# Optimization experiments

Measured on AMD Instinct MI355X. Metric: run time of the kernel, lower is better.

The kernel has to match this reference:

```python
import jax, jax.numpy as jnp
import numpy as np

N = 131072        # active input voxels (= output voxels for submanifold conv)
KVOL = 27         # 3x3x3 kernel volume
P = 65536         # neighbor pairs per kernel offset (regularized kernel map)
CIN = 64
COUT = 64


def setup_inputs() -> dict:
    key = jax.random.key(0)
    k1, k2, k3, k4, k5 = jax.random.split(key, 5)
    in_feats = jax.random.normal(k1, (N, CIN), dtype=jnp.float32)
    kernel = jax.random.normal(k2, (KVOL, CIN, COUT), dtype=jnp.float32) * (1.0 / np.sqrt(CIN * KVOL))
    bias_param = jax.random.normal(k3, (COUT,), dtype=jnp.float32)
    imap = jax.random.randint(k4, (KVOL, P), 0, N, dtype=jnp.int32)
    omap = jax.random.randint(k5, (KVOL, P), 0, N, dtype=jnp.int32)
    return {"in_feats": in_feats, "kernel": kernel, "bias_param": bias_param,
            "imap": imap, "omap": omap}


def reference(in_feats, kernel, bias_param, imap, omap):
    # Sparse 3D conv as gather -> per-offset GEMM -> scatter-add.
    # gathered: [KVOL, P, CIN]
    gathered = in_feats[imap]
    # per-offset GEMM: [KVOL, P, COUT]
    contrib = jnp.einsum('kpc,kco->kpo', gathered, kernel)
    out = jnp.zeros((N, COUT), dtype=in_feats.dtype)
    out = out.at[omap.reshape(-1)].add(contrib.reshape(-1, COUT))
    out = out + bias_param
    return out
```

## Files before the change

kernel.cpp:

```cpp
#include <hip/hip_runtime.h>
#include <hip/hip_bf16.h>
#include <stdint.h>

#define N_VOX 131072
#define KVOL  27
#define PPK   65536
#define CIN   64
#define COUT  64
#define TOT   (KVOL * PPK)
#define SORT_BLOCKS 864
#define GEMM_BLOCKS (KVOL * (PPK / 128))
#define NB    512

typedef __attribute__((ext_vector_type(8))) short short8;
typedef __attribute__((ext_vector_type(4))) float f32x4;

#define SCAN512(s, tid)                                       \
  for (int off = 1; off < 512; off <<= 1) {                   \
    int va_ = ((tid) >= off) ? s[(tid) - off] : 0;            \
    int vb_ = (((tid) + 256) >= off) ? s[(tid) + 256 - off] : 0; \
    __syncthreads();                                          \
    s[(tid)] += va_; s[(tid) + 256] += vb_;                   \
    __syncthreads();                                          \
  }

__device__ __forceinline__ void gl_lds16(const void* g, void* l) {
  __builtin_amdgcn_global_load_lds(
      (const __attribute__((address_space(1))) unsigned int*)g,
      (__attribute__((address_space(3))) unsigned int*)l,
      16, 0, 0);
}

__device__ __forceinline__ unsigned short f2bf(float f) {
  __hip_bfloat16 h = __float2bfloat16(f);
  return *reinterpret_cast<unsigned short*>(&h);
}


__global__ __launch_bounds__(256) void prep_hist_kernel(
    const float* __restrict__ in, unsigned short* __restrict__ inb,
    const float* __restrict__ w, unsigned short* __restrict__ wt,
    const int* __restrict__ omap, int* __restrict__ counts, int do_sort) {
  int b = blockIdx.x;
  if (do_sort) {
    if (b < SORT_BLOCKS) {
      __shared__ unsigned int hist[NB];
      int tid = threadIdx.x;
      hist[tid] = 0; hist[tid + 256] = 0;
      __syncthreads();
      int e0 = (b * 256 + tid) * 8;
      int4 o0 = *(const int4*)(omap + e0);
      int4 o1 = *(const int4*)(omap + e0 + 4);
      atomicAdd(&hist[(unsigned)o0.x >> 8], 1u);
      atomicAdd(&hist[(unsigned)o0.y >> 8], 1u);
      atomicAdd(&hist[(unsigned)o0.z >> 8], 1u);
      atomicAdd(&hist[(unsigned)o0.w >> 8], 1u);
      atomicAdd(&hist[(unsigned)o1.x >> 8], 1u);
      atomicAdd(&hist[(unsigned)o1.y >> 8], 1u);
      atomicAdd(&hist[(unsigned)o1.z >> 8], 1u);
      atomicAdd(&hist[(unsigned)o1.w >> 8], 1u);
      __syncthreads();
      counts[(size_t)b * NB + tid]       = (int)hist[tid];
      counts[(size_t)b * NB + tid + 256] = (int)hist[tid + 256];
      return;
    }
    b -= SORT_BLOCKS;
  }
  if (b < 4096) {
    int i = b * 256 + threadIdx.x;
    const float4* in4 = (const float4*)in;
    float4 f0 = in4[2 * i], f1 = in4[2 * i + 1];
    union { unsigned short u[8]; short8 v; } r;
    r.u[0] = f2bf(f0.x); r.u[1] = f2bf(f0.y); r.u[2] = f2bf(f0.z); r.u[3] = f2bf(f0.w);
    r.u[4] = f2bf(f1.x); r.u[5] = f2bf(f1.y); r.u[6] = f2bf(f1.z); r.u[7] = f2bf(f1.w);
    ((short8*)inb)[i] = r.v;
  } else {
    int k = b - 4096;
    const float* wk = w + k * CIN * COUT;
    unsigned short* wtk = wt + k * CIN * COUT;
    for (int idx = threadIdx.x; idx < CIN * COUT; idx += 256) {
      int c = idx >> 6, o = idx & 63;
      wtk[o * 64 + c] = f2bf(wk[idx]);
    }
  }
}


__global__ __launch_bounds__(256) void scan_blocks_kernel(
    const int* __restrict__ counts, int* __restrict__ blockbase,
    int* __restrict__ totals) {
  __shared__ int s[256];
  int b = blockIdx.x, t = threadIdx.x;
  int c0 = 0, c1 = 0, c2 = 0, c3 = 0;
  if (t < 216) {
    c0 = counts[(size_t)(4 * t + 0) * NB + b];
    c1 = counts[(size_t)(4 * t + 1) * NB + b];
    c2 = counts[(size_t)(4 * t + 2) * NB + b];
    c3 = counts[(size_t)(4 * t + 3) * NB + b];
  }
  int sum = c0 + c1 + c2 + c3;
  s[t] = sum; __syncthreads();
  for (int off = 1; off < 256; off <<= 1) {
    int v = (t >= off) ? s[t - off] : 0;
    __syncthreads();
    s[t] += v;
    __syncthreads();
  }
  int excl = s[t] - sum;
  int* brow = blockbase + (size_t)b * SORT_BLOCKS;
  if (t < 216) {
    brow[t * 4]     = excl;
    brow[t * 4 + 1] = excl + c0;
    brow[t * 4 + 2] = excl + c0 + c1;
    brow[t * 4 + 3] = excl + c0 + c1 + c2;
  }
  if (t == 255) totals[b] = s[255];
}


__global__ __launch_bounds__(256) void scatter_kernel(
    const int* __restrict__ omap, const int* __restrict__ blockbase,
    const int* __restrict__ totals, unsigned int* __restrict__ pairs) {
  __shared__ int ts[NB];
  __shared__ unsigned int gb[NB];
  __shared__ unsigned int cur[NB];
  int b = blockIdx.x, tid = threadIdx.x;
  int t0 = totals[tid], t1 = totals[tid + 256];
  ts[tid] = t0; ts[tid + 256] = t1;
  __syncthreads();
  SCAN512(ts, tid);
  gb[tid]       = (unsigned)(ts[tid] - t0 +
                    blockbase[(size_t)tid * SORT_BLOCKS + b]);
  gb[tid + 256] = (unsigned)(ts[tid + 256] - t1 +
                    blockbase[(size_t)(tid + 256) * SORT_BLOCKS + b]);
  cur[tid] = 0; cur[tid + 256] = 0;
  __syncthreads();
  int e0 = (b * 256 + tid) * 8;
  int4 o0 = *(const int4*)(omap + e0);
  int4 o1 = *(const int4*)(omap + e0 + 4);
  unsigned int key[8] = {(unsigned)o0.x, (unsigned)o0.y, (unsigned)o0.z, (unsigned)o0.w,
                         (unsigned)o1.x, (unsigned)o1.y, (unsigned)o1.z, (unsigned)o1.w};
#pragma unroll
  for (int i = 0; i < 8; i++) {
    unsigned int bk = key[i] >> 8;
    unsigned int r = atomicAdd(&cur[bk], 1u);
    unsigned int pos = gb[bk] + r;
    pairs[pos] = (((unsigned)(e0 + i)) << 8) | (key[i] & 255u);
  }
}


__global__ __launch_bounds__(256) void refine_kernel(
    const unsigned int* __restrict__ pairs, const int* __restrict__ totals,
    int* __restrict__ islotf, int* __restrict__ ofs, int* __restrict__ cnt) {
  __shared__ int ts[NB];
  __shared__ unsigned int hist[256];
  __shared__ unsigned int scn[256];
  __shared__ unsigned int cur[256];
  int b = blockIdx.x, t = threadIdx.x;
  int t0 = totals[t], t1 = totals[t + 256];
  ts[t] = t0; ts[t + 256] = t1;
  hist[t] = 0;
  __syncthreads();
  SCAN512(ts, t);
  __shared__ int sb_s, n_s;
  if (t == 0) { n_s = totals[b]; sb_s = ts[b] - n_s; }
  __syncthreads();
  int sb = sb_s, n = n_s;

  for (int i = t; i < n; i += 256)
    atomicAdd(&hist[pairs[sb + i] & 255u], 1u);
  __syncthreads();
  unsigned int h = hist[t];
  scn[t] = h;
  __syncthreads();
  for (int off = 1; off < 256; off <<= 1) {
    unsigned int v = (t >= off) ? scn[t - off] : 0;
    __syncthreads();
    scn[t] += v;
    __syncthreads();
  }
  unsigned int excl = scn[t] - h;
  ofs[b * 256 + t] = sb + (int)excl;
  cnt[b * 256 + t] = (int)h;
  cur[t] = excl;
  __syncthreads();
  for (int i = t; i < n; i += 256) {
    unsigned int v = pairs[sb + i];
    unsigned int r = atomicAdd(&cur[v & 255u], 1u);
    islotf[v >> 8] = sb + (int)r;
  }
}


__global__ __launch_bounds__(256) void spconv_store_kernel(
    const unsigned short* __restrict__ inb,
    const unsigned short* __restrict__ wt,
    const int* __restrict__ imap,
    const int* __restrict__ islotf,
    unsigned short* __restrict__ contrib) {
  __shared__ __align__(16) char smem[24576];
  short* A_lds = (short*)smem;
  short* B_lds = (short*)(smem + 16384);
  short* C_sh  = (short*)smem;
  __shared__ int perm_s[128];

  int bid = blockIdx.x;
  int k = bid >> 9;
  int pbase = (bid & 511) * 128;
  int tid = threadIdx.x;
  int wave = tid >> 6, lane = tid & 63;
  int m = lane & 15, q = lane >> 4;

  const int* imk = imap + k * PPK;
  const unsigned short* wtk = wt + k * 4096;

  if (tid < 128) perm_s[tid] = islotf[k * PPK + pbase + tid];

#pragma unroll
  for (int i = 0; i < 2; i++) {
    int id = wave * 2 + i;
    int t = id >> 1, s = id & 1;
    const unsigned short* g = wtk + (t * 16 + m) * 64 + s * 32 + q * 8;
    gl_lds16(g, &B_lds[(t * 128 + s * 64) * 8]);
  }
#pragma unroll
  for (int j = 0; j < 2; j++) {
    int r = wave * 2 + j;
    int row = imk[pbase + r * 16 + m];
    const unsigned short* g0 = inb + row * 64 + q * 8;
    gl_lds16(g0,      &A_lds[(r * 128)      * 8]);
    gl_lds16(g0 + 32, &A_lds[(r * 128 + 64) * 8]);
  }
  __syncthreads();

  const short8* Af = (const short8*)A_lds;
  const short8* Bf = (const short8*)B_lds;

  short8 a[2][2], b[4][2];
#pragma unroll
  for (int r2 = 0; r2 < 2; r2++) {
    int r = wave * 2 + r2;
#pragma unroll
    for (int s = 0; s < 2; s++) a[r2][s] = Af[r * 128 + s * 64 + lane];
  }
#pragma unroll
  for (int t = 0; t < 4; t++)
#pragma unroll
    for (int s = 0; s < 2; s++) b[t][s] = Bf[t * 128 + s * 64 + lane];

  __syncthreads();

  f32x4 acc[2][4];
#pragma unroll
  for (int r2 = 0; r2 < 2; r2++)
#pragma unroll
    for (int t = 0; t < 4; t++) {
      f32x4 c = {0.f, 0.f, 0.f, 0.f};
      c = __builtin_amdgcn_mfma_f32_16x16x32_bf16(a[r2][0], b[t][0], c, 0, 0, 0);
      c = __builtin_amdgcn_mfma_f32_16x16x32_bf16(a[r2][1], b[t][1], c, 0, 0, 0);
      acc[r2][t] = c;
    }

#pragma unroll
  for (int r2 = 0; r2 < 2; r2++) {
    int pl = (wave * 2 + r2) * 16 + q * 4;
#pragma unroll
    for (int t = 0; t < 4; t++)
#pragma unroll
      for (int reg = 0; reg < 4; reg++)
        C_sh[(pl + reg) * 72 + t * 16 + m] = (short)f2bf(acc[r2][t][reg]);
  }
  __syncthreads();

#pragma unroll
  for (int i = 0; i < 4; i++) {
    int id = i * 256 + tid;
    int row = id >> 3, ch = (id & 7) * 8;
    short8 v = *(const short8*)&C_sh[row * 72 + ch];
    *((short8*)&contrib[(size_t)perm_s[row] * 64 + ch]) = v;
  }
}


__global__ __launch_bounds__(256) void reduce_kernel(
    const unsigned short* __restrict__ contrib,
    const int* __restrict__ ofs,
    const int* __restrict__ cnt,
    const float* __restrict__ bias,
    float* __restrict__ out) {
  int row = blockIdx.x * 4 + (threadIdx.x >> 6);
  int lane = threadIdx.x & 63;
  int rg = lane >> 3, ch = (lane & 7) * 8;
  int s = ofs[row], n = cnt[row];

  float acc[8];
#pragma unroll
  for (int i = 0; i < 8; i++) acc[i] = 0.f;

  int j = rg;
  for (; j + 8 < n; j += 16) {
    short8 v0 = __builtin_nontemporal_load((const short8*)&contrib[(size_t)(s + j) * 64 + ch]);
    short8 v1 = __builtin_nontemporal_load((const short8*)&contrib[(size_t)(s + j + 8) * 64 + ch]);
#pragma unroll
    for (int i = 0; i < 8; i++)
      acc[i] += __uint_as_float((unsigned int)(unsigned short)v0[i] << 16);
#pragma unroll
    for (int i = 0; i < 8; i++)
      acc[i] += __uint_as_float((unsigned int)(unsigned short)v1[i] << 16);
  }
  if (j < n) {
    short8 v0 = __builtin_nontemporal_load((const short8*)&contrib[(size_t)(s + j) * 64 + ch]);
#pragma unroll
    for (int i = 0; i < 8; i++)
      acc[i] += __uint_as_float((unsigned int)(unsigned short)v0[i] << 16);
  }

#pragma unroll
  for (int mask = 8; mask < 64; mask <<= 1)
#pragma unroll
    for (int i = 0; i < 8; i++) acc[i] += __shfl_xor(acc[i], mask, 64);

  if (rg == 0) {
    float4 b0 = *(const float4*)(bias + ch);
    float4 b1 = *(const float4*)(bias + ch + 4);
    float4 r0 = {acc[0] + b0.x, acc[1] + b0.y, acc[2] + b0.z, acc[3] + b0.w};
    float4 r1 = {acc[4] + b1.x, acc[5] + b1.y, acc[6] + b1.z, acc[7] + b1.w};
    *(float4*)(out + (size_t)row * 64 + ch) = r0;
    *(float4*)(out + (size_t)row * 64 + ch + 4) = r1;
  }
}


__global__ __launch_bounds__(256) void init_out_kernel(float* __restrict__ out,
                                                       const float* __restrict__ bias) {
  int i = blockIdx.x * blockDim.x + threadIdx.x;
  float4 b = *(const float4*)(bias + ((i * 4) & 63));
  ((float4*)out)[i] = b;
}

__global__ __launch_bounds__(256) void spconv_atomic_kernel(
    const unsigned short* __restrict__ inb,
    const unsigned short* __restrict__ wt,
    const int* __restrict__ imap, const int* __restrict__ omap,
    float* __restrict__ out) {
  __shared__ __align__(16) short A_lds[128 * 64];
  __shared__ __align__(16) short B_lds[64 * 64];

  int bid = blockIdx.x;
  int k = bid >> 9;
  int pbase = (bid & 511) * 128;
  int tid = threadIdx.x;
  int wave = tid >> 6, lane = tid & 63;
  int m = lane & 15, q = lane >> 4;

  const int* imk = imap + k * PPK;
  const int* omk = omap + k * PPK;
  const unsigned short* wtk = wt + k * 4096;

#pragma unroll
  for (int i = 0; i < 2; i++) {
    int id = wave * 2 + i;
    int t = id >> 1, s = id & 1;
    const unsigned short* g = wtk + (t * 16 + m) * 64 + s * 32 + q * 8;
    gl_lds16(g, &B_lds[(t * 128 + s * 64) * 8]);
  }
#pragma unroll
  for (int j = 0; j < 2; j++) {
    int r = wave * 2 + j;
    int row = imk[pbase + r * 16 + m];
    const unsigned short* g0 = inb + row * 64 + q * 8;
    gl_lds16(g0,      &A_lds[(r * 128)      * 8]);
    gl_lds16(g0 + 32, &A_lds[(r * 128 + 64) * 8]);
  }
  __syncthreads();

  const short8* Af = (const short8*)A_lds;
  const short8* Bf = (const short8*)B_lds;
  short8 a[2][2], b[4][2];
#pragma unroll
  for (int r2 = 0; r2 < 2; r2++) {
    int r = wave * 2 + r2;
#pragma unroll
    for (int s = 0; s < 2; s++) a[r2][s] = Af[r * 128 + s * 64 + lane];
  }
#pragma unroll
  for (int t = 0; t < 4; t++)
#pragma unroll
    for (int s = 0; s < 2; s++) b[t][s] = Bf[t * 128 + s * 64 + lane];

  f32x4 acc[2][4];
#pragma unroll
  for (int r2 = 0; r2 < 2; r2++)
#pragma unroll
    for (int t = 0; t < 4; t++) {
      f32x4 c = {0.f, 0.f, 0.f, 0.f};
      c = __builtin_amdgcn_mfma_f32_16x16x32_bf16(a[r2][0], b[t][0], c, 0, 0, 0);
      c = __builtin_amdgcn_mfma_f32_16x16x32_bf16(a[r2][1], b[t][1], c, 0, 0, 0);
      acc[r2][t] = c;
    }

  int orow[2][4];
#pragma unroll
  for (int r2 = 0; r2 < 2; r2++) {
    int pr = pbase + (wave * 2 + r2) * 16 + q * 4;
#pragma unroll
    for (int reg = 0; reg < 4; reg++) orow[r2][reg] = omk[pr + reg];
  }
#pragma unroll
  for (int r2 = 0; r2 < 2; r2++)
#pragma unroll
    for (int t = 0; t < 4; t++)
#pragma unroll
      for (int reg = 0; reg < 4; reg++)
        atomicAdd(out + (size_t)orow[r2][reg] * 64 + t * 16 + m, acc[r2][t][reg]);
}


extern "C" void kernel_launch(void* const* d_in, const int* in_sizes, int n_in,
                              void* d_out, int out_size, void* d_ws, size_t ws_size,
                              hipStream_t stream) {
  const float* in_feats = (const float*)d_in[0];
  const float* kern     = (const float*)d_in[1];
  const float* bias     = (const float*)d_in[2];
  const int*   imap     = (const int*)d_in[3];
  const int*   omap     = (const int*)d_in[4];
  float* out = (float*)d_out;

  char* ws = (char*)d_ws;
  size_t off = 0;
  auto alloc = [&](size_t bytes) { size_t o = off; off = (off + bytes + 255) & ~(size_t)255; return o; };

  size_t o_inb   = alloc((size_t)N_VOX * CIN * 2);
  size_t o_wt    = alloc((size_t)KVOL * CIN * COUT * 2);
  size_t o_cts   = alloc((size_t)NB * SORT_BLOCKS * 4);
  size_t o_bb    = alloc((size_t)NB * SORT_BLOCKS * 4);
  size_t o_tot   = alloc((size_t)NB * 4);
  size_t o_islot = alloc((size_t)TOT * 4);
  size_t o_ctb   = alloc((size_t)TOT * 64 * 2);
  size_t needed = off;

  unsigned short* inb = (unsigned short*)(ws + o_inb);
  unsigned short* wt  = (unsigned short*)(ws + o_wt);
  int* counts    = (int*)(ws + o_cts);
  int* blockbase = (int*)(ws + o_bb);
  int* totals    = (int*)(ws + o_tot);
  int* islotf    = (int*)(ws + o_islot);
  unsigned short* ctb = (unsigned short*)(ws + o_ctb);
  unsigned int* pairs = (unsigned int*)(ws + o_ctb);
  int* ofs = (int*)(ws + o_cts);
  int* cnt = ofs + N_VOX;

  bool fast = (ws_size >= needed);

  if (fast) {
    prep_hist_kernel<<<SORT_BLOCKS + 4096 + KVOL, 256, 0, stream>>>(
        in_feats, inb, kern, wt, omap, counts, 1);
    scan_blocks_kernel<<<NB, 256, 0, stream>>>(counts, blockbase, totals);
    scatter_kernel<<<SORT_BLOCKS, 256, 0, stream>>>(omap, blockbase, totals, pairs);
    refine_kernel<<<NB, 256, 0, stream>>>(pairs, totals, islotf, ofs, cnt);
    spconv_store_kernel<<<GEMM_BLOCKS, 256, 0, stream>>>(inb, wt, imap, islotf, ctb);
    reduce_kernel<<<N_VOX / 4, 256, 0, stream>>>(ctb, ofs, cnt, bias, out);
  } else {
    prep_hist_kernel<<<4096 + KVOL, 256, 0, stream>>>(
        in_feats, inb, kern, wt, omap, nullptr, 0);
    init_out_kernel<<<(N_VOX * COUT / 4) / 256, 256, 0, stream>>>(out, bias);
    spconv_atomic_kernel<<<GEMM_BLOCKS, 256, 0, stream>>>(inb, wt, imap, omap, out);
  }
}
```

Measured before the change: 258.0 us.

## Fuse counting-sort stages into one cooperative kernel with grid syncs

Merges the four sort-related launches (histogram+convert, block scan, scatter, refine) into a single cooperative kernel of 512 persistent blocks separated by grid.sync barriers. The goal is to remove per-launch overhead and inter-kernel gaps, and to compute the bucket prefix sums once per block instead of recomputing them in separate kernels. In exchange, grid-stride loops run with fewer blocks than before, so the histogram, convert and scatter phases have less parallelism. Grid-wide barriers also add their own cost, and the cooperative launch requires all 512 blocks to be co-resident.

Result: slower. 475.4 us (+84.2%).

```diff
diff --git a/kernel.cpp b/kernel.cpp
--- a/kernel.cpp
+++ b/kernel.cpp
@@ -1,6 +1,9 @@
 #include <hip/hip_runtime.h>
+#include <hip/hip_cooperative_groups.h>
 #include <hip/hip_bf16.h>
 #include <stdint.h>
+
+namespace cg = cooperative_groups;
 
 #define N_VOX 131072
 #define KVOL  27
@@ -11,6 +14,7 @@
 #define SORT_BLOCKS 864
 #define GEMM_BLOCKS (KVOL * (PPK / 128))
 #define NB    512
+#define CGRID 512
 
 typedef __attribute__((ext_vector_type(8))) short short8;
 typedef __attribute__((ext_vector_type(4))) float f32x4;
@@ -37,158 +41,151 @@
 }
 
 
-__global__ __launch_bounds__(256) void prep_hist_kernel(
+__global__ __launch_bounds__(256) void sort_coop_kernel(
     const float* __restrict__ in, unsigned short* __restrict__ inb,
     const float* __restrict__ w, unsigned short* __restrict__ wt,
-    const int* __restrict__ omap, int* __restrict__ counts, int do_sort) {
-  int b = blockIdx.x;
-  if (do_sort) {
-    if (b < SORT_BLOCKS) {
-      __shared__ unsigned int hist[NB];
-      int tid = threadIdx.x;
-      hist[tid] = 0; hist[tid + 256] = 0;
-      __syncthreads();
-      int e0 = (b * 256 + tid) * 8;
+    const int* __restrict__ omap,
+    int* __restrict__ counts, int* __restrict__ blockbase,
+    int* __restrict__ totals, unsigned int* __restrict__ pairs,
+    int* __restrict__ islotf, int* __restrict__ ofs, int* __restrict__ cnt) {
+  cg::grid_group grid = cg::this_grid();
+  int tid = threadIdx.x;
+
+  __shared__ unsigned int histA[NB];
+  __shared__ int s256[256];
+  __shared__ int ts[NB];
+  __shared__ int bbs[NB];
+  __shared__ unsigned int gb[NB];
+  __shared__ unsigned int cur[NB];
+  __shared__ unsigned int h256[256];
+  __shared__ unsigned int scn[256];
+  __shared__ unsigned int curD[256];
+
+  for (int u = blockIdx.x; u < SORT_BLOCKS + 4096 + KVOL; u += CGRID) {
+    if (u < SORT_BLOCKS) {
+      histA[tid] = 0; histA[tid + 256] = 0;
+      __syncthreads();
+      int e0 = (u * 256 + tid) * 8;
       int4 o0 = *(const int4*)(omap + e0);
       int4 o1 = *(const int4*)(omap + e0 + 4);
-      atomicAdd(&hist[(unsigned)o0.x >> 8], 1u);
-      atomicAdd(&hist[(unsigned)o0.y >> 8], 1u);
-      atomicAdd(&hist[(unsigned)o0.z >> 8], 1u);
-      atomicAdd(&hist[(unsigned)o0.w >> 8], 1u);
-      atomicAdd(&hist[(unsigned)o1.x >> 8], 1u);
-      atomicAdd(&hist[(unsigned)o1.y >> 8], 1u);
-      atomicAdd(&hist[(unsigned)o1.z >> 8], 1u);
-      atomicAdd(&hist[(unsigned)o1.w >> 8], 1u);
-      __syncthreads();
-      counts[(size_t)b * NB + tid]       = (int)hist[tid];
-      counts[(size_t)b * NB + tid + 256] = (int)hist[tid + 256];
-      return;
-    }
-    b -= SORT_BLOCKS;
-  }
-  if (b < 4096) {
-    int i = b * 256 + threadIdx.x;
-    const float4* in4 = (const float4*)in;
-    float4 f0 = in4[2 * i], f1 = in4[2 * i + 1];
-    union { unsigned short u[8]; short8 v; } r;
-    r.u[0] = f2bf(f0.x); r.u[1] = f2bf(f0.y); r.u[2] = f2bf(f0.z); r.u[3] = f2bf(f0.w);
-    r.u[4] = f2bf(f1.x); r.u[5] = f2bf(f1.y); r.u[6] = f2bf(f1.z); r.u[7] = f2bf(f1.w);
-    ((short8*)inb)[i] = r.v;
-  } else {
-    int k = b - 4096;
-    const float* wk = w + k * CIN * COUT;
-    unsigned short* wtk = wt + k * CIN * COUT;
-    for (int idx = threadIdx.x; idx < CIN * COUT; idx += 256) {
-      int c = idx >> 6, o = idx & 63;
-      wtk[o * 64 + c] = f2bf(wk[idx]);
-    }
-  }
-}
-
-
-__global__ __launch_bounds__(256) void scan_blocks_kernel(
-    const int* __restrict__ counts, int* __restrict__ blockbase,
-    int* __restrict__ totals) {
-  __shared__ int s[256];
-  int b = blockIdx.x, t = threadIdx.x;
-  int c0 = 0, c1 = 0, c2 = 0, c3 = 0;
-  if (t < 216) {
-    c0 = counts[(size_t)(4 * t + 0) * NB + b];
-    c1 = counts[(size_t)(4 * t + 1) * NB + b];
-    c2 = counts[(size_t)(4 * t + 2) * NB + b];
-    c3 = counts[(size_t)(4 * t + 3) * NB + b];
-  }
-  int sum = c0 + c1 + c2 + c3;
-  s[t] = sum; __syncthreads();
-  for (int off = 1; off < 256; off <<= 1) {
-    int v = (t >= off) ? s[t - off] : 0;
-    __syncthreads();
-    s[t] += v;
-    __syncthreads();
-  }
-  int excl = s[t] - sum;
-  int* brow = blockbase + (size_t)b * SORT_BLOCKS;
-  if (t < 216) {
-    brow[t * 4]     = excl;
-    brow[t * 4 + 1] = excl + c0;
-    brow[t * 4 + 2] = excl + c0 + c1;
-    brow[t * 4 + 3] = excl + c0 + c1 + c2;
-  }
-  if (t == 255) totals[b] = s[255];
-}
-
-
-__global__ __launch_bounds__(256) void scatter_kernel(
-    const int* __restrict__ omap, const int* __restrict__ blockbase,
-    const int* __restrict__ totals, unsigned int* __restrict__ pairs) {
-  __shared__ int ts[NB];
-  __shared__ unsigned int gb[NB];
-  __shared__ unsigned int cur[NB];
-  int b = blockIdx.x, tid = threadIdx.x;
-  int t0 = totals[tid], t1 = totals[tid + 256];
-  ts[tid] = t0; ts[tid + 256] = t1;
+      atomicAdd(&histA[(unsigned)o0.x >> 8], 1u);
+      atomicAdd(&histA[(unsigned)o0.y >> 8], 1u);
+      atomicAdd(&histA[(unsigned)o0.z >> 8], 1u);
+      atomicAdd(&histA[(unsigned)o0.w >> 8], 1u);
+      atomicAdd(&histA[(unsigned)o1.x >> 8], 1u);
+      atomicAdd(&histA[(unsigned)o1.y >> 8], 1u);
+      atomicAdd(&histA[(unsigned)o1.z >> 8], 1u);
+      atomicAdd(&histA[(unsigned)o1.w >> 8], 1u);
+      __syncthreads();
+      counts[(size_t)u * NB + tid]       = (int)histA[tid];
+      counts[(size_t)u * NB + tid + 256] = (int)histA[tid + 256];
+      __syncthreads();
+    } else if (u < SORT_BLOCKS + 4096) {
+      int i = (u - SORT_BLOCKS) * 256 + tid;
+      const float4* in4 = (const float4*)in;
+      float4 f0 = in4[2 * i], f1 = in4[2 * i + 1];
+      union { unsigned short us[8]; short8 v; } r;
+      r.us[0] = f2bf(f0.x); r.us[1] = f2bf(f0.y); r.us[2] = f2bf(f0.z); r.us[3] = f2bf(f0.w);
+      r.us[4] = f2bf(f1.x); r.us[5] = f2bf(f1.y); r.us[6] = f2bf(f1.z); r.us[7] = f2bf(f1.w);
+      ((short8*)inb)[i] = r.v;
+    } else {
+      int k = u - SORT_BLOCKS - 4096;
+      const float* wk = w + k * CIN * COUT;
+      unsigned short* wtk = wt + k * CIN * COUT;
+      for (int idx = tid; idx < CIN * COUT; idx += 256) {
+        int c = idx >> 6, o = idx & 63;
+        wtk[o * 64 + c] = f2bf(wk[idx]);
+      }
+    }
+  }
+  grid.sync();
+
+  {
+    int b = blockIdx.x;
+    int c0 = 0, c1 = 0, c2 = 0, c3 = 0;
+    if (tid < 216) {
+      c0 = counts[(size_t)(4 * tid + 0) * NB + b];
+      c1 = counts[(size_t)(4 * tid + 1) * NB + b];
+      c2 = counts[(size_t)(4 * tid + 2) * NB + b];
+      c3 = counts[(size_t)(4 * tid + 3) * NB + b];
+    }
+    int sum = c0 + c1 + c2 + c3;
+    s256[tid] = sum; __syncthreads();
+    for (int off = 1; off < 256; off <<= 1) {
+      int v = (tid >= off) ? s256[tid - off] : 0;
+      __syncthreads();
+      s256[tid] += v;
+      __syncthreads();
+    }
+    int excl = s256[tid] - sum;
+    int* brow = blockbase + (size_t)b * SORT_BLOCKS;
+    if (tid < 216) {
+      brow[tid * 4]     = excl;
+      brow[tid * 4 + 1] = excl + c0;
+      brow[tid * 4 + 2] = excl + c0 + c1;
+      brow[tid * 4 + 3] = excl + c0 + c1 + c2;
+    }
+    if (tid == 255) totals[b] = s256[255];
+  }
+  grid.sync();
+
+  int t0v = totals[tid], t1v = totals[tid + 256];
+  ts[tid] = t0v; ts[tid + 256] = t1v;
   __syncthreads();
   SCAN512(ts, tid);
-  gb[tid]       = (unsigned)(ts[tid] - t0 +
-                    blockbase[(size_t)tid * SORT_BLOCKS + b]);
-  gb[tid + 256] = (unsigned)(ts[tid + 256] - t1 +
-                    blockbase[(size_t)(tid + 256) * SORT_BLOCKS + b]);
-  cur[tid] = 0; cur[tid + 256] = 0;
-  __syncthreads();
-  int e0 = (b * 256 + tid) * 8;
-  int4 o0 = *(const int4*)(omap + e0);
-  int4 o1 = *(const int4*)(omap + e0 + 4);
-  unsigned int key[8] = {(unsigned)o0.x, (unsigned)o0.y, (unsigned)o0.z, (unsigned)o0.w,
-                         (unsigned)o1.x, (unsigned)o1.y, (unsigned)o1.z, (unsigned)o1.w};
-#pragma unroll
-  for (int i = 0; i < 8; i++) {
-    unsigned int bk = key[i] >> 8;
-    unsigned int r = atomicAdd(&cur[bk], 1u);
-    unsigned int pos = gb[bk] + r;
-    pairs[pos] = (((unsigned)(e0 + i)) << 8) | (key[i] & 255u);
-  }
-}
-
-
-__global__ __launch_bounds__(256) void refine_kernel(
-    const unsigned int* __restrict__ pairs, const int* __restrict__ totals,
-    int* __restrict__ islotf, int* __restrict__ ofs, int* __restrict__ cnt) {
-  __shared__ int ts[NB];
-  __shared__ unsigned int hist[256];
-  __shared__ unsigned int scn[256];
-  __shared__ unsigned int cur[256];
-  int b = blockIdx.x, t = threadIdx.x;
-  int t0 = totals[t], t1 = totals[t + 256];
-  ts[t] = t0; ts[t + 256] = t1;
-  hist[t] = 0;
-  __syncthreads();
-  SCAN512(ts, t);
-  __shared__ int sb_s, n_s;
-  if (t == 0) { n_s = totals[b]; sb_s = ts[b] - n_s; }
-  __syncthreads();
-  int sb = sb_s, n = n_s;
-
-  for (int i = t; i < n; i += 256)
-    atomicAdd(&hist[pairs[sb + i] & 255u], 1u);
-  __syncthreads();
-  unsigned int h = hist[t];
-  scn[t] = h;
-  __syncthreads();
-  for (int off = 1; off < 256; off <<= 1) {
-    unsigned int v = (t >= off) ? scn[t - off] : 0;
-    __syncthreads();
-    scn[t] += v;
-    __syncthreads();
-  }
-  unsigned int excl = scn[t] - h;
-  ofs[b * 256 + t] = sb + (int)excl;
-  cnt[b * 256 + t] = (int)h;
-  cur[t] = excl;
-  __syncthreads();
-  for (int i = t; i < n; i += 256) {
-    unsigned int v = pairs[sb + i];
-    unsigned int r = atomicAdd(&cur[v & 255u], 1u);
-    islotf[v >> 8] = sb + (int)r;
+  int bb0 = ts[tid] - t0v;
+  int bb1 = ts[tid + 256] - t1v;
+  bbs[tid] = bb0; bbs[tid + 256] = bb1;
+  __syncthreads();
+  for (int u = blockIdx.x; u < SORT_BLOCKS; u += CGRID) {
+    gb[tid]       = (unsigned)(bb0 + blockbase[(size_t)tid * SORT_BLOCKS + u]);
+    gb[tid + 256] = (unsigned)(bb1 + blockbase[(size_t)(tid + 256) * SORT_BLOCKS + u]);
+    cur[tid] = 0; cur[tid + 256] = 0;
+    __syncthreads();
+    int e0 = (u * 256 + tid) * 8;
+    int4 o0 = *(const int4*)(omap + e0);
+    int4 o1 = *(const int4*)(omap + e0 + 4);
+    unsigned int key[8] = {(unsigned)o0.x, (unsigned)o0.y, (unsigned)o0.z, (unsigned)o0.w,
+                           (unsigned)o1.x, (unsigned)o1.y, (unsigned)o1.z, (unsigned)o1.w};
+#pragma unroll
+    for (int i = 0; i < 8; i++) {
+      unsigned int bk = key[i] >> 8;
+      unsigned int r = atomicAdd(&cur[bk], 1u);
+      unsigned int pos = gb[bk] + r;
+      pairs[pos] = (((unsigned)(e0 + i)) << 8) | (key[i] & 255u);
+    }
+    __syncthreads();
+  }
+  grid.sync();
+
+  {
+    int b = blockIdx.x;
+    int sb = bbs[b];
+    int n = totals[b];
+    h256[tid] = 0;
+    __syncthreads();
+    for (int i = tid; i < n; i += 256)
+      atomicAdd(&h256[pairs[sb + i] & 255u], 1u);
+    __syncthreads();
+    unsigned int h = h256[tid];
+    scn[tid] = h;
+    __syncthreads();
+    for (int off = 1; off < 256; off <<= 1) {
+      unsigned int v = (tid >= off) ? scn[tid - off] : 0;
+      __syncthreads();
+      scn[tid] += v;
+      __syncthreads();
+    }
+    unsigned int excl = scn[tid] - h;
+    ofs[b * 256 + tid] = sb + (int)excl;
+    cnt[b * 256 + tid] = (int)h;
+    curD[tid] = excl;
+    __syncthreads();
+    for (int i = tid; i < n; i += 256) {
+      unsigned int v = pairs[sb + i];
+      unsigned int r = atomicAdd(&curD[v & 255u], 1u);
+      islotf[v >> 8] = sb + (int)r;
+    }
   }
 }
 
@@ -332,6 +329,29 @@
 }
 
 
+__global__ __launch_bounds__(256) void prep_fallback_kernel(
+    const float* __restrict__ in, unsigned short* __restrict__ inb,
+    const float* __restrict__ w, unsigned short* __restrict__ wt) {
+  int b = blockIdx.x;
+  if (b < 4096) {
+    int i = b * 256 + threadIdx.x;
+    const float4* in4 = (const float4*)in;
+    float4 f0 = in4[2 * i], f1 = in4[2 * i + 1];
+    union { unsigned short us[8]; short8 v; } r;
+    r.us[0] = f2bf(f0.x); r.us[1] = f2bf(f0.y); r.us[2] = f2bf(f0.z); r.us[3] = f2bf(f0.w);
+    r.us[4] = f2bf(f1.x); r.us[5] = f2bf(f1.y); r.us[6] = f2bf(f1.z); r.us[7] = f2bf(f1.w);
+    ((short8*)inb)[i] = r.v;
+  } else {
+    int k = b - 4096;
+    const float* wk = w + k * CIN * COUT;
+    unsigned short* wtk = wt + k * CIN * COUT;
+    for (int idx = threadIdx.x; idx < CIN * COUT; idx += 256) {
+      int c = idx >> 6, o = idx & 63;
+      wtk[o * 64 + c] = f2bf(wk[idx]);
+    }
+  }
+}
+
 __global__ __launch_bounds__(256) void init_out_kernel(float* __restrict__ out,
                                                        const float* __restrict__ bias) {
   int i = blockIdx.x * blockDim.x + threadIdx.x;
@@ -454,16 +474,16 @@
   bool fast = (ws_size >= needed);
 
   if (fast) {
-    prep_hist_kernel<<<SORT_BLOCKS + 4096 + KVOL, 256, 0, stream>>>(
-        in_feats, inb, kern, wt, omap, counts, 1);
-    scan_blocks_kernel<<<NB, 256, 0, stream>>>(counts, blockbase, totals);
-    scatter_kernel<<<SORT_BLOCKS, 256, 0, stream>>>(omap, blockbase, totals, pairs);
-    refine_kernel<<<NB, 256, 0, stream>>>(pairs, totals, islotf, ofs, cnt);
+    void* cargs[] = {(void*)&in_feats, (void*)&inb, (void*)&kern, (void*)&wt,
+                     (void*)&omap, (void*)&counts, (void*)&blockbase,
+                     (void*)&totals, (void*)&pairs, (void*)&islotf,
+                     (void*)&ofs, (void*)&cnt};
+    (void)hipLaunchCooperativeKernel((const void*)sort_coop_kernel,
+                                     dim3(CGRID), dim3(256), cargs, 0, stream);
     spconv_store_kernel<<<GEMM_BLOCKS, 256, 0, stream>>>(inb, wt, imap, islotf, ctb);
     reduce_kernel<<<N_VOX / 4, 256, 0, stream>>>(ctb, ofs, cnt, bias, out);
   } else {
-    prep_hist_kernel<<<4096 + KVOL, 256, 0, stream>>>(
-        in_feats, inb, kern, wt, omap, nullptr, 0);
+    prep_fallback_kernel<<<4096 + KVOL, 256, 0, stream>>>(in_feats, inb, kern, wt);
     init_out_kernel<<<(N_VOX * COUT / 4) / 256, 256, 0, stream>>>(out, bias);
     spconv_atomic_kernel<<<GEMM_BLOCKS, 256, 0, stream>>>(inb, wt, imap, omap, out);
   }
```
